# Kernel optimization log

Measured on AMD Instinct MI355X. Metric: run time of the kernel, lower is better.

## Reference

```python
import jax, jax.numpy as jnp
import numpy as np

N_NODES = 50000
N_EDGES = 800000
IN_NODE = 64
IN_EDGE = 32
HIDDEN = 128
NUM_LAYERS = 3
OUT_DIM = 8
NUM_GRAPHS = 128


def setup_inputs() -> dict:
    key = jax.random.key(0)
    ks = jax.random.split(key, 20)
    inp = {
        "x": jax.random.normal(ks[0], (N_NODES, IN_NODE), dtype=jnp.float32),
        "edge_index": jax.random.randint(ks[1], (2, N_EDGES), 0, N_NODES, dtype=jnp.int32),
        "edge_attr": jax.random.normal(ks[2], (N_EDGES, IN_EDGE), dtype=jnp.float32),
        "batch": jnp.sort(jax.random.randint(ks[3], (N_NODES,), 0, NUM_GRAPHS, dtype=jnp.int32)),
    }
    # MLP params per GINEConv layer: Linear(d_in, H) -> ReLU -> Linear(H, H)
    d_ins = [IN_NODE + IN_EDGE] + [HIDDEN + IN_EDGE] * (NUM_LAYERS - 1)
    for i, d_in in enumerate(d_ins):
        inp[f"w{i}_1"] = jax.random.normal(ks[4 + 3 * i], (d_in, HIDDEN), dtype=jnp.float32) * (1.0 / np.sqrt(d_in))
        inp[f"b{i}_1"] = jnp.zeros((HIDDEN,), dtype=jnp.float32)
        inp[f"w{i}_2"] = jax.random.normal(ks[5 + 3 * i], (HIDDEN, HIDDEN), dtype=jnp.float32) * (1.0 / np.sqrt(HIDDEN))
        inp[f"b{i}_2"] = jnp.zeros((HIDDEN,), dtype=jnp.float32)
    inp["lin_w"] = jax.random.normal(ks[15], (HIDDEN, OUT_DIM), dtype=jnp.float32) * (1.0 / np.sqrt(HIDDEN))
    inp["lin_b"] = jnp.zeros((OUT_DIM,), dtype=jnp.float32)
    return inp


def _gine_conv(x, src, dst, edge_attr, w1, b1, w2, b2):
    # gather source node feats, concat with edge feats, 2-layer MLP, scatter-add to dst
    m = jnp.concatenate([x[src], edge_attr], axis=-1)        # [E, d_in]
    h = jax.nn.relu(m @ w1 + b1) @ w2 + b2                   # [E, H]
    return jax.ops.segment_sum(h, dst, num_segments=N_NODES)  # [N, H]


def reference(x, edge_index, edge_attr, batch,
              w0_1, b0_1, w0_2, b0_2,
              w1_1, b1_1, w1_2, b1_2,
              w2_1, b2_1, w2_2, b2_2,
              lin_w, lin_b):
    src, dst = edge_index[0], edge_index[1]
    layers = [(w0_1, b0_1, w0_2, b0_2), (w1_1, b1_1, w1_2, b1_2), (w2_1, b2_1, w2_2, b2_2)]
    h = x
    for (w1, b1, w2, b2) in layers:
        h = jax.nn.relu(_gine_conv(h, src, dst, edge_attr, w1, b1, w2, b2))
    # global mean pool over graphs
    sums = jax.ops.segment_sum(h, batch, num_segments=NUM_GRAPHS)          # [G, H]
    cnts = jax.ops.segment_sum(jnp.ones((N_NODES,), h.dtype), batch, num_segments=NUM_GRAPHS)
    pooled = sums / jnp.maximum(cnts, 1.0)[:, None]
    return pooled @ lin_w + lin_b
```

## Files before the change

kernel.cpp:

```cpp
#include <hip/hip_runtime.h>
#include <hip/hip_bf16.h>
#include <stdint.h>

typedef __attribute__((ext_vector_type(8))) __bf16 bf16x8;
typedef __attribute__((ext_vector_type(4))) __bf16 bf16x4;
typedef __attribute__((ext_vector_type(4))) float f32x4;

static constexpr int NN = 50000;
static constexpr int NE = 800000;
static constexpr int FX = 64;
static constexpr int FE = 32;
static constexpr int H  = 128;
static constexpr int NG = 128;
static constexpr int OD = 8;

__global__ void cvt_f32_bf16(const float* __restrict__ in, __bf16* __restrict__ out, int n) {
  int idx = (blockIdx.x * blockDim.x + threadIdx.x) * 4;
  if (idx + 3 < n) {
    float4 v = *reinterpret_cast<const float4*>(in + idx);
    bf16x4 o;
    o[0] = (__bf16)v.x; o[1] = (__bf16)v.y; o[2] = (__bf16)v.z; o[3] = (__bf16)v.w;
    *reinterpret_cast<bf16x4*>(out + idx) = o;
  } else {
    for (; idx < n; ++idx) out[idx] = (__bf16)in[idx];
  }
}

__global__ void cvt_w_t(const float* __restrict__ w, __bf16* __restrict__ wt, int K) {
  int i = blockIdx.x * blockDim.x + threadIdx.x;
  if (i >= K * 128) return;
  int n = i / K, k = i % K;
  wt[i] = (__bf16)w[k * 128 + n];
}

__global__ void hist_build(const int* __restrict__ dst, int* __restrict__ hist) {
  int e = blockIdx.x * blockDim.x + threadIdx.x;
  if (e < NE) atomicAdd(&hist[dst[e]], 1);
}

__global__ void scan1(const int* __restrict__ hist, int* __restrict__ excl, int* __restrict__ btot) {
  __shared__ int tmp[256];
  int t = threadIdx.x;
  int i = blockIdx.x * 256 + t;
  int v = (i < NN) ? hist[i] : 0;
  tmp[t] = v;
  __syncthreads();
  for (int off = 1; off < 256; off <<= 1) {
    int add = (t >= off) ? tmp[t - off] : 0;
    __syncthreads();
    tmp[t] += add;
    __syncthreads();
  }
  if (i < NN) excl[i] = tmp[t] - v;
  if (t == 255) btot[blockIdx.x] = tmp[255];
}

__global__ void scan2(int* __restrict__ btot, int nb) {
  __shared__ int tmp[256];
  int t = threadIdx.x;
  int v = (t < nb) ? btot[t] : 0;
  tmp[t] = v;
  __syncthreads();
  for (int off = 1; off < 256; off <<= 1) {
    int add = (t >= off) ? tmp[t - off] : 0;
    __syncthreads();
    tmp[t] += add;
    __syncthreads();
  }
  if (t < nb) btot[t] = tmp[t] - v;
}

__global__ void scan3(const int* __restrict__ excl, const int* __restrict__ btot,
                      int* __restrict__ cursor) {
  int i = blockIdx.x * 256 + threadIdx.x;
  if (i < NN) cursor[i] = excl[i] + btot[blockIdx.x];
}

__global__ void scatter_perm(const int* __restrict__ src, const int* __restrict__ dst,
                             int* __restrict__ cursor,
                             int* __restrict__ srcp, int* __restrict__ dstp,
                             int* __restrict__ eperm) {
  int e = blockIdx.x * blockDim.x + threadIdx.x;
  if (e >= NE) return;
  int d = dst[e];
  int p = atomicAdd(&cursor[d], 1);
  srcp[p] = src[e];
  dstp[p] = d;
  eperm[p] = e;
}

__global__ void sort_ea(const float* __restrict__ ea, const int* __restrict__ eperm,
                        __bf16* __restrict__ eabs) {
  int i = blockIdx.x * blockDim.x + threadIdx.x;
  if (i >= NE * 4) return;
  int p = i >> 2, c = i & 3;
  int e = eperm[p];
  float4 v0 = *reinterpret_cast<const float4*>(ea + (size_t)e * FE + c * 8);
  float4 v1 = *reinterpret_cast<const float4*>(ea + (size_t)e * FE + c * 8 + 4);
  bf16x8 o;
  o[0] = (__bf16)v0.x; o[1] = (__bf16)v0.y; o[2] = (__bf16)v0.z; o[3] = (__bf16)v0.w;
  o[4] = (__bf16)v1.x; o[5] = (__bf16)v1.y; o[6] = (__bf16)v1.z; o[7] = (__bf16)v1.w;
  *reinterpret_cast<bf16x8*>(eabs + (size_t)p * FE + c * 8) = o;
}

template<int F, int DIN>
__global__ __launch_bounds__(512) void node_gemm2(
    const __bf16* __restrict__ Ain,
    const __bf16* __restrict__ wt,
    __bf16* __restrict__ Y)
{
  constexpr int APAD = F + 8;
  constexpr int KS   = F / 32;
  constexpr int CH   = F / 8;
  constexpr int AB   = 128 * APAD * 2;
  constexpr int OB   = 128 * 136 * 2;
  constexpr int SB   = (AB > OB) ? AB : OB;
  __shared__ __align__(16) char smem[SB];
  auto As  = reinterpret_cast<__bf16 (*)[APAD]>(smem);
  auto Ost = reinterpret_cast<__bf16 (*)[136]>(smem);

  const int tid   = threadIdx.x;
  const int lane  = tid & 63;
  const int w     = tid >> 6;
  const int m0    = blockIdx.x * 128;
  const int colq  = lane & 15;
  const int krow  = (lane >> 4) * 8;
  const int rbase = (lane >> 4) * 4;
  const int col   = w * 16 + colq;

  bf16x8 bf[KS];
#pragma unroll
  for (int ks = 0; ks < KS; ++ks)
    bf[ks] = *reinterpret_cast<const bf16x8*>(wt + (size_t)col * DIN + ks * 32 + krow);

  for (int i = tid; i < 128 * CH; i += 512) {
    int row = i / CH, c = i % CH;
    int g = m0 + row; if (g >= NN) g = NN - 1;
    *reinterpret_cast<bf16x8*>(&As[row][c * 8]) =
        *reinterpret_cast<const bf16x8*>(Ain + (size_t)g * F + c * 8);
  }
  __syncthreads();

  f32x4 acc[8];
#pragma unroll
  for (int mt = 0; mt < 8; ++mt) acc[mt] = (f32x4){0.f, 0.f, 0.f, 0.f};
#pragma unroll
  for (int ks = 0; ks < KS; ++ks)
#pragma unroll
    for (int mt = 0; mt < 8; ++mt) {
      bf16x8 a = *reinterpret_cast<const bf16x8*>(&As[mt * 16 + colq][ks * 32 + krow]);
      acc[mt] = __builtin_amdgcn_mfma_f32_16x16x32_bf16(a, bf[ks], acc[mt], 0, 0, 0);
    }
  __syncthreads();

#pragma unroll
  for (int mt = 0; mt < 8; ++mt)
#pragma unroll
    for (int r = 0; r < 4; ++r)
      Ost[mt * 16 + rbase + r][col] = (__bf16)acc[mt][r];
  __syncthreads();

  for (int i = tid; i < 128 * 16; i += 512) {
    int row = i >> 4, c = i & 15;
    int g = m0 + row;
    if (g < NN)
      *reinterpret_cast<bf16x8*>(Y + (size_t)g * H + c * 8) =
          *reinterpret_cast<const bf16x8*>(&Ost[row][c * 8]);
  }
}

template<bool WRITE_Y>
__global__ __launch_bounds__(512) void node_wy(
    const float* __restrict__ aggHin,
    const int* __restrict__ deg,
    const __bf16* __restrict__ w2t,
    const float* __restrict__ b2,
    const __bf16* __restrict__ w1t,
    __bf16* __restrict__ Y,
    float* __restrict__ hpre)
{
  __shared__ __bf16 Ast[128][136];
  __shared__ __bf16 Hst[WRITE_Y ? 128 : 1][136];
  __shared__ int deg_s[128];

  const int tid   = threadIdx.x;
  const int lane  = tid & 63;
  const int w     = tid >> 6;
  const int m0    = blockIdx.x * 128;
  const int colq  = lane & 15;
  const int krow  = (lane >> 4) * 8;
  const int rbase = (lane >> 4) * 4;
  const int col   = w * 16 + colq;

  for (int i = tid; i < 128 * 16; i += 512) {
    int row = i >> 4, cb = (i & 15) * 8;
    int g = m0 + row; if (g >= NN) g = NN - 1;
    const float* s = aggHin + (size_t)g * H + cb;
    float4 v0 = *reinterpret_cast<const float4*>(s);
    float4 v1 = *reinterpret_cast<const float4*>(s + 4);
    bf16x8 o;
    o[0] = (__bf16)v0.x; o[1] = (__bf16)v0.y; o[2] = (__bf16)v0.z; o[3] = (__bf16)v0.w;
    o[4] = (__bf16)v1.x; o[5] = (__bf16)v1.y; o[6] = (__bf16)v1.z; o[7] = (__bf16)v1.w;
    *reinterpret_cast<bf16x8*>(&Ast[row][cb]) = o;
  }
  if (tid < 128) {
    int g = m0 + tid;
    deg_s[tid] = (g < NN) ? deg[g] : 0;
  }
  __syncthreads();

  bf16x8 w2f[4];
#pragma unroll
  for (int ks = 0; ks < 4; ++ks)
    w2f[ks] = *reinterpret_cast<const bf16x8*>(w2t + (size_t)col * H + ks * 32 + krow);
  const float b2s = b2[col];

  f32x4 acc[8];
#pragma unroll
  for (int mt = 0; mt < 8; ++mt) acc[mt] = (f32x4){0.f, 0.f, 0.f, 0.f};
#pragma unroll
  for (int ks = 0; ks < 4; ++ks)
#pragma unroll
    for (int mt = 0; mt < 8; ++mt) {
      bf16x8 a = *reinterpret_cast<const bf16x8*>(&Ast[mt * 16 + colq][ks * 32 + krow]);
      acc[mt] = __builtin_amdgcn_mfma_f32_16x16x32_bf16(a, w2f[ks], acc[mt], 0, 0, 0);
    }

  if (WRITE_Y) {
#pragma unroll
    for (int mt = 0; mt < 8; ++mt)
#pragma unroll
      for (int r = 0; r < 4; ++r) {
        int row = mt * 16 + rbase + r;
        float v = acc[mt][r] + (float)deg_s[row] * b2s;
        Hst[row][col] = (__bf16)fmaxf(v, 0.f);
      }
    __syncthreads();

    bf16x8 w1f[4];
#pragma unroll
    for (int ks = 0; ks < 4; ++ks)
      w1f[ks] = *reinterpret_cast<const bf16x8*>(w1t + (size_t)col * 160 + ks * 32 + krow);

    f32x4 acc2[8];
#pragma unroll
    for (int mt = 0; mt < 8; ++mt) acc2[mt] = (f32x4){0.f, 0.f, 0.f, 0.f};
#pragma unroll
    for (int ks = 0; ks < 4; ++ks)
#pragma unroll
      for (int mt = 0; mt < 8; ++mt) {
        bf16x8 a = *reinterpret_cast<const bf16x8*>(&Hst[mt * 16 + colq][ks * 32 + krow]);
        acc2[mt] = __builtin_amdgcn_mfma_f32_16x16x32_bf16(a, w1f[ks], acc2[mt], 0, 0, 0);
      }

#pragma unroll
    for (int mt = 0; mt < 8; ++mt)
#pragma unroll
      for (int r = 0; r < 4; ++r)
        Ast[mt * 16 + rbase + r][col] = (__bf16)acc2[mt][r];
    __syncthreads();

    for (int i = tid; i < 128 * 16; i += 512) {
      int row = i >> 4, cb = (i & 15) * 8;
      int g = m0 + row;
      if (g < NN)
        *reinterpret_cast<bf16x8*>(Y + (size_t)g * H + cb) =
            *reinterpret_cast<const bf16x8*>(&Ast[row][cb]);
    }
  } else {
#pragma unroll
    for (int mt = 0; mt < 8; ++mt)
#pragma unroll
      for (int r = 0; r < 4; ++r) {
        int row = mt * 16 + rbase + r;
        int g = m0 + row;
        if (g < NN)
          hpre[(size_t)g * H + col] = acc[mt][r] + (float)deg_s[row] * b2s;
      }
  }
}

template<int DIN>
__global__ __launch_bounds__(512) void edge_mlp4(
    const __bf16* __restrict__ Yb,
    const __bf16* __restrict__ eabs,
    const int* __restrict__ srcp, const int* __restrict__ dstp,
    const __bf16* __restrict__ w1t,
    const float* __restrict__ b1,
    float* __restrict__ aggH,
    int ntiles)
{
  constexpr int F = DIN - 32;
  constexpr int TPB = 4;
  __shared__ __bf16 Ylds[128][128];
  __shared__ int dst_s[128];

  const int tid   = threadIdx.x;
  const int lane  = tid & 63;
  const int w     = tid >> 6;
  const int colq  = lane & 15;
  const int krow  = (lane >> 4) * 8;
  const int rbase = (lane >> 4) * 4;
  const int col   = w * 16 + colq;

  const bf16x8 b1f = *reinterpret_cast<const bf16x8*>(w1t + (size_t)col * DIN + F + krow);
  const float  b1s = b1[col];

  const int yrow = tid >> 4;
  const int yc   = tid & 15;
  const int drow = tid & 127;

  int t0 = blockIdx.x * TPB;
  int t1 = t0 + TPB; if (t1 > ntiles) t1 = ntiles;
  if (t0 >= ntiles) return;

  int e0 = t0 * 128;
  int sA[4];
#pragma unroll
  for (int k = 0; k < 4; ++k) sA[k] = srcp[e0 + yrow + 32 * k];
  int dreg = dstp[e0 + drow];
  bf16x8 yreg[4];
#pragma unroll
  for (int k = 0; k < 4; ++k)
    yreg[k] = *reinterpret_cast<const bf16x8*>(Yb + (size_t)sA[k] * H + yc * 8);
  bf16x8 aef[8];
#pragma unroll
  for (int mt = 0; mt < 8; ++mt)
    aef[mt] = *reinterpret_cast<const bf16x8*>(eabs + (size_t)(e0 + mt * 16 + colq) * FE + krow);
  {
    int e0n = (t0 + 1 < t1) ? (t0 + 1) * 128 : e0;
#pragma unroll
    for (int k = 0; k < 4; ++k) sA[k] = srcp[e0n + yrow + 32 * k];
  }

  for (int t = t0; t < t1; ++t) {
    __syncthreads();
#pragma unroll
    for (int k = 0; k < 4; ++k) {
      int row = yrow + 32 * k;
      int cb = (yc * 8 + ((row >> 2) & 3) * 16) & 127;
      *reinterpret_cast<bf16x8*>(&Ylds[row][cb]) = yreg[k];
    }
    if (tid < 128) dst_s[tid] = dreg;
    __syncthreads();

    if (t + 1 < t1) {
      int e1 = (t + 1) * 128;
#pragma unroll
      for (int k = 0; k < 4; ++k)
        yreg[k] = *reinterpret_cast<const bf16x8*>(Yb + (size_t)sA[k] * H + yc * 8);
      dreg = dstp[e1 + drow];
      int e2 = (t + 2 < t1) ? (t + 2) * 128 : e1;
#pragma unroll
      for (int k = 0; k < 4; ++k) sA[k] = srcp[e2 + yrow + 32 * k];
    }

    f32x4 acc[8];
#pragma unroll
    for (int mt = 0; mt < 8; ++mt) acc[mt] = (f32x4){b1s, b1s, b1s, b1s};
#pragma unroll
    for (int mt = 0; mt < 8; ++mt)
      acc[mt] = __builtin_amdgcn_mfma_f32_16x16x32_bf16(aef[mt], b1f, acc[mt], 0, 0, 0);

    if (t + 1 < t1) {
      int e1 = (t + 1) * 128;
#pragma unroll
      for (int mt = 0; mt < 8; ++mt)
        aef[mt] = *reinterpret_cast<const bf16x8*>(eabs + (size_t)(e1 + mt * 16 + colq) * FE + krow);
    }

#pragma unroll
    for (int mt = 0; mt < 8; ++mt)
#pragma unroll
      for (int r = 0; r < 4; ++r) {
        int row = mt * 16 + rbase + r;
        int cs = (col + ((row >> 2) & 3) * 16) & 127;
        float v = (float)Ylds[row][cs] + acc[mt][r];
        Ylds[row][cs] = (__bf16)fmaxf(v, 0.f);
      }
    __syncthreads();

    {
      const int rc = tid & 127;
      const int r0 = (tid >> 7) * 32;
      float s = 0.f;
      int d = dst_s[r0];
#pragma unroll 4
      for (int r = r0; r < r0 + 32; ++r) {
        int dn = dst_s[r];
        float v = (float)Ylds[r][(rc + ((r >> 2) & 3) * 16) & 127];
        if (dn != d) { atomicAdd(aggH + (size_t)d * H + rc, s); s = 0.f; d = dn; }
        s += v;
      }
      atomicAdd(aggH + (size_t)d * H + rc, s);
    }
  }
}

__global__ void pool_kernel(const float* __restrict__ agg, const int* __restrict__ batch,
                            float* __restrict__ sums, float* __restrict__ cnts) {
  const int col = threadIdx.x & 127;
  const int sub = threadIdx.x >> 7;
  const int NB = 128;
  int n0 = blockIdx.x * NB + sub * (NB / 2);
  if (n0 >= NN) return;
  int n1 = n0 + NB / 2; if (n1 > NN) n1 = NN;
  float s = 0.f, c = 0.f;
  int g = batch[n0];
  for (int n = n0; n < n1; ++n) {
    int gn = batch[n];
    if (gn != g) {
      atomicAdd(&sums[g * H + col], s);
      if (col == 0) atomicAdd(&cnts[g], c);
      s = 0.f; c = 0.f; g = gn;
    }
    s += fmaxf(agg[(size_t)n * H + col], 0.f);
    c += 1.f;
  }
  atomicAdd(&sums[g * H + col], s);
  if (col == 0) atomicAdd(&cnts[g], c);
}

__global__ void final_kernel(const float* __restrict__ sums, const float* __restrict__ cnts,
                             const float* __restrict__ lw, const float* __restrict__ lb,
                             float* __restrict__ out) {
  int idx = blockIdx.x * blockDim.x + threadIdx.x;
  if (idx >= NG * OD) return;
  int g = idx / OD, o = idx % OD;
  float inv = 1.f / fmaxf(cnts[g], 1.f);
  float s = 0.f;
#pragma unroll 8
  for (int k = 0; k < H; ++k)
    s += sums[g * H + k] * lw[k * OD + o];
  out[idx] = s * inv + lb[o];
}

extern "C" void kernel_launch(void* const* d_in, const int* in_sizes, int n_in,
                              void* d_out, int out_size, void* d_ws, size_t ws_size,
                              hipStream_t stream) {
  const float* x   = (const float*)d_in[0];
  const int*   ei  = (const int*)d_in[1];
  const float* ea  = (const float*)d_in[2];
  const int*   bat = (const int*)d_in[3];
  const float* w1[3] = {(const float*)d_in[4], (const float*)d_in[8],  (const float*)d_in[12]};
  const float* b1[3] = {(const float*)d_in[5], (const float*)d_in[9],  (const float*)d_in[13]};
  const float* w2[3] = {(const float*)d_in[6], (const float*)d_in[10], (const float*)d_in[14]};
  const float* b2[3] = {(const float*)d_in[7], (const float*)d_in[11], (const float*)d_in[15]};
  const float* lw  = (const float*)d_in[16];
  const float* lb  = (const float*)d_in[17];
  float* out = (float*)d_out;

  char* ws = (char*)d_ws;
  size_t off = 0;
  auto alloc = [&](size_t bytes) -> void* {
    void* p = ws + off;
    off = (off + bytes + 255) & ~(size_t)255;
    return p;
  };
  __bf16* xb   = (__bf16*)alloc((size_t)NN * FX * 2);
  __bf16* Yb   = (__bf16*)alloc((size_t)NN * H * 2);
  __bf16* eabs = (__bf16*)alloc((size_t)NE * FE * 2);
  float*  agg  = (float*) alloc((size_t)NN * H * 4);
  __bf16* w1t[3]; __bf16* w2t[3];
  for (int l = 0; l < 3; ++l) {
    w1t[l] = (__bf16*)alloc(128 * 160 * 2);
    w2t[l] = (__bf16*)alloc(128 * 128 * 2);
  }
  float* sums = (float*)alloc(NG * H * 4);
  float* cnts = (float*)alloc(NG * 4);
  int* hist   = (int*)alloc((size_t)NN * 4);
  int* excl   = (int*)alloc((size_t)NN * 4);
  int* btot   = (int*)alloc(256 * 4);
  int* cursor = (int*)alloc((size_t)NN * 4);
  int* srcp   = (int*)alloc((size_t)NE * 4);
  int* dstp   = (int*)alloc((size_t)NE * 4);
  int* eperm  = (int*)alloc((size_t)NE * 4);

  const int* src = ei;
  const int* dst = ei + NE;
  const int NB_SCAN = (NN + 255) / 256;
  const int NTILES = NE / 128;
  const int EGRID  = (NTILES + 3) / 4;
  const int NGRID  = (NN + 127) / 128;

  cvt_f32_bf16<<<(NN * FX / 4 + 255) / 256, 256, 0, stream>>>(x, xb, NN * FX);
  const int dins[3] = {96, 160, 160};
  for (int l = 0; l < 3; ++l) {
    cvt_w_t<<<(dins[l] * 128 + 255) / 256, 256, 0, stream>>>(w1[l], w1t[l], dins[l]);
    cvt_w_t<<<(128 * 128 + 255) / 256, 256, 0, stream>>>(w2[l], w2t[l], 128);
  }

  hipMemsetAsync(hist, 0, (size_t)NN * 4, stream);
  hist_build<<<(NE + 255) / 256, 256, 0, stream>>>(dst, hist);
  scan1<<<NB_SCAN, 256, 0, stream>>>(hist, excl, btot);
  scan2<<<1, 256, 0, stream>>>(btot, NB_SCAN);
  scan3<<<NB_SCAN, 256, 0, stream>>>(excl, btot, cursor);
  scatter_perm<<<(NE + 255) / 256, 256, 0, stream>>>(src, dst, cursor, srcp, dstp, eperm);
  sort_ea<<<(NE * 4 + 255) / 256, 256, 0, stream>>>(ea, eperm, eabs);

  node_gemm2<64, 96><<<NGRID, 512, 0, stream>>>(xb, w1t[0], Yb);
  hipMemsetAsync(agg, 0, (size_t)NN * H * 4, stream);
  edge_mlp4<96><<<EGRID, 512, 0, stream>>>(Yb, eabs, srcp, dstp, w1t[0], b1[0], agg, NTILES);

  for (int l = 1; l < 3; ++l) {
    node_wy<true><<<NGRID, 512, 0, stream>>>(agg, hist, w2t[l - 1], b2[l - 1],
                                             w1t[l], Yb, nullptr);
    hipMemsetAsync(agg, 0, (size_t)NN * H * 4, stream);
    edge_mlp4<160><<<EGRID, 512, 0, stream>>>(Yb, eabs, srcp, dstp, w1t[l], b1[l], agg, NTILES);
  }

  node_wy<false><<<NGRID, 512, 0, stream>>>(agg, hist, w2t[2], b2[2],
                                            nullptr, nullptr, agg);
  hipMemsetAsync(sums, 0, NG * H * 4, stream);
  hipMemsetAsync(cnts, 0, NG * 4, stream);
  pool_kernel<<<(NN + 127) / 128, 256, 0, stream>>>(agg, bat, sums, cnts);
  final_kernel<<<(NG * OD + 255) / 256, 256, 0, stream>>>(sums, cnts, lw, lb, out);
}
```

Baseline: 481.4 us.

## Partition edge MLP by destination node ranges with LDS-local aggregation

Replaces the fixed edge-tile partition with a CSR rowptr-based split where each block owns 32 destination nodes and processes all of their incoming edges. Partial sums are reduced in shared memory with LDS atomics and written once to global memory. This removes the global float atomics and the per-layer memset of the aggregation buffer. The cost is load imbalance across blocks (variable edge counts), a larger LDS footprint that may reduce occupancy, and removal of the Ylds swizzle (padding to 132 used instead).

```diff
diff --git a/kernel.cpp b/kernel.cpp
--- a/kernel.cpp
+++ b/kernel.cpp
@@ -13,6 +13,7 @@
 static constexpr int H  = 128;
 static constexpr int NG = 128;
 static constexpr int OD = 8;
+static constexpr int NPB = 32;
 
 __global__ void cvt_f32_bf16(const float* __restrict__ in, __bf16* __restrict__ out, int n) {
   int idx = (blockIdx.x * blockDim.x + threadIdx.x) * 4;
@@ -71,9 +72,14 @@
 }
 
 __global__ void scan3(const int* __restrict__ excl, const int* __restrict__ btot,
-                      int* __restrict__ cursor) {
+                      int* __restrict__ cursor, int* __restrict__ rowptr) {
   int i = blockIdx.x * 256 + threadIdx.x;
-  if (i < NN) cursor[i] = excl[i] + btot[blockIdx.x];
+  if (i < NN) {
+    int v = excl[i] + btot[blockIdx.x];
+    cursor[i] = v;
+    rowptr[i] = v;
+  }
+  if (blockIdx.x == 0 && threadIdx.x == 0) rowptr[NN] = NE;
 }
 
 __global__ void scatter_perm(const int* __restrict__ src, const int* __restrict__ dst,
@@ -281,19 +287,19 @@
 }
 
 template<int DIN>
-__global__ __launch_bounds__(512) void edge_mlp4(
+__global__ __launch_bounds__(512) void edge_mlp5(
     const __bf16* __restrict__ Yb,
     const __bf16* __restrict__ eabs,
     const int* __restrict__ srcp, const int* __restrict__ dstp,
+    const int* __restrict__ rowptr,
     const __bf16* __restrict__ w1t,
     const float* __restrict__ b1,
-    float* __restrict__ aggH,
-    int ntiles)
+    float* __restrict__ aggH)
 {
   constexpr int F = DIN - 32;
-  constexpr int TPB = 4;
-  __shared__ __bf16 Ylds[128][128];
-  __shared__ int dst_s[128];
+  __shared__ __bf16 Ylds[128][132];
+  __shared__ float  agg_l[33][132];
+  __shared__ int    nl_s[128];
 
   const int tid   = threadIdx.x;
   const int lane  = tid & 63;
@@ -303,6 +309,15 @@
   const int rbase = (lane >> 4) * 4;
   const int col   = w * 16 + colq;
 
+  const int nb0 = blockIdx.x * NPB;
+  const int nb1 = (nb0 + NPB < NN) ? nb0 + NPB : NN;
+  const int eb0 = rowptr[nb0];
+  const int eb1 = rowptr[nb1];
+  const int ntb = (eb1 - eb0 + 127) >> 7;
+
+  for (int i = tid; i < 33 * 132; i += 512)
+    (&agg_l[0][0])[i] = 0.f;
+
   const bf16x8 b1f = *reinterpret_cast<const bf16x8*>(w1t + (size_t)col * DIN + F + krow);
   const float  b1s = b1[col];
 
@@ -310,90 +325,123 @@
   const int yc   = tid & 15;
   const int drow = tid & 127;
 
-  int t0 = blockIdx.x * TPB;
-  int t1 = t0 + TPB; if (t1 > ntiles) t1 = ntiles;
-  if (t0 >= ntiles) return;
-
-  int e0 = t0 * 128;
-  int sA[4];
-#pragma unroll
-  for (int k = 0; k < 4; ++k) sA[k] = srcp[e0 + yrow + 32 * k];
-  int dreg = dstp[e0 + drow];
-  bf16x8 yreg[4];
-#pragma unroll
-  for (int k = 0; k < 4; ++k)
-    yreg[k] = *reinterpret_cast<const bf16x8*>(Yb + (size_t)sA[k] * H + yc * 8);
-  bf16x8 aef[8];
-#pragma unroll
-  for (int mt = 0; mt < 8; ++mt)
-    aef[mt] = *reinterpret_cast<const bf16x8*>(eabs + (size_t)(e0 + mt * 16 + colq) * FE + krow);
-  {
-    int e0n = (t0 + 1 < t1) ? (t0 + 1) * 128 : e0;
-#pragma unroll
-    for (int k = 0; k < 4; ++k) sA[k] = srcp[e0n + yrow + 32 * k];
-  }
-
-  for (int t = t0; t < t1; ++t) {
-    __syncthreads();
+  if (ntb > 0) {
+    int sA[4];
 #pragma unroll
     for (int k = 0; k < 4; ++k) {
-      int row = yrow + 32 * k;
-      int cb = (yc * 8 + ((row >> 2) & 3) * 16) & 127;
-      *reinterpret_cast<bf16x8*>(&Ylds[row][cb]) = yreg[k];
-    }
-    if (tid < 128) dst_s[tid] = dreg;
-    __syncthreads();
-
-    if (t + 1 < t1) {
-      int e1 = (t + 1) * 128;
+      int e = eb0 + yrow + 32 * k; if (e > NE - 1) e = NE - 1;
+      sA[k] = srcp[e];
+    }
+    int dreg;
+    { int e = eb0 + drow; if (e > NE - 1) e = NE - 1; dreg = dstp[e]; }
+    bf16x8 yreg[4];
+#pragma unroll
+    for (int k = 0; k < 4; ++k)
+      yreg[k] = *reinterpret_cast<const bf16x8*>(Yb + (size_t)sA[k] * H + yc * 8);
+    bf16x8 aef[8];
+#pragma unroll
+    for (int mt = 0; mt < 8; ++mt) {
+      int e = eb0 + mt * 16 + colq; if (e > NE - 1) e = NE - 1;
+      aef[mt] = *reinterpret_cast<const bf16x8*>(eabs + (size_t)e * FE + krow);
+    }
+    {
+      int e1 = eb0 + ((1 < ntb) ? 128 : 0);
+#pragma unroll
+      for (int k = 0; k < 4; ++k) {
+        int e = e1 + yrow + 32 * k; if (e > NE - 1) e = NE - 1;
+        sA[k] = srcp[e];
+      }
+    }
+
+    for (int t = 0; t < ntb; ++t) {
+      __syncthreads();
 #pragma unroll
       for (int k = 0; k < 4; ++k)
-        yreg[k] = *reinterpret_cast<const bf16x8*>(Yb + (size_t)sA[k] * H + yc * 8);
-      dreg = dstp[e1 + drow];
-      int e2 = (t + 2 < t1) ? (t + 2) * 128 : e1;
-#pragma unroll
-      for (int k = 0; k < 4; ++k) sA[k] = srcp[e2 + yrow + 32 * k];
-    }
-
-    f32x4 acc[8];
-#pragma unroll
-    for (int mt = 0; mt < 8; ++mt) acc[mt] = (f32x4){b1s, b1s, b1s, b1s};
-#pragma unroll
-    for (int mt = 0; mt < 8; ++mt)
-      acc[mt] = __builtin_amdgcn_mfma_f32_16x16x32_bf16(aef[mt], b1f, acc[mt], 0, 0, 0);
-
-    if (t + 1 < t1) {
-      int e1 = (t + 1) * 128;
+        *reinterpret_cast<bf16x8*>(&Ylds[yrow + 32 * k][yc * 8]) = yreg[k];
+      if (tid < 128) {
+        int e = eb0 + t * 128 + tid;
+        nl_s[tid] = (e < eb1) ? (dreg - nb0) : 32;
+      }
+      __syncthreads();
+
+      if (t + 1 < ntb) {
+        int e1 = eb0 + (t + 1) * 128;
+#pragma unroll
+        for (int k = 0; k < 4; ++k)
+          yreg[k] = *reinterpret_cast<const bf16x8*>(Yb + (size_t)sA[k] * H + yc * 8);
+        { int e = e1 + drow; if (e > NE - 1) e = NE - 1; dreg = dstp[e]; }
+        int e2 = eb0 + ((t + 2 < ntb) ? (t + 2) : (t + 1)) * 128;
+#pragma unroll
+        for (int k = 0; k < 4; ++k) {
+          int e = e2 + yrow + 32 * k; if (e > NE - 1) e = NE - 1;
+          sA[k] = srcp[e];
+        }
+      }
+
+      f32x4 acc[8];
+#pragma unroll
+      for (int mt = 0; mt < 8; ++mt) acc[mt] = (f32x4){b1s, b1s, b1s, b1s};
 #pragma unroll
       for (int mt = 0; mt < 8; ++mt)
-        aef[mt] = *reinterpret_cast<const bf16x8*>(eabs + (size_t)(e1 + mt * 16 + colq) * FE + krow);
-    }
-
-#pragma unroll
-    for (int mt = 0; mt < 8; ++mt)
-#pragma unroll
-      for (int r = 0; r < 4; ++r) {
-        int row = mt * 16 + rbase + r;
-        int cs = (col + ((row >> 2) & 3) * 16) & 127;
-        float v = (float)Ylds[row][cs] + acc[mt][r];
-        Ylds[row][cs] = (__bf16)fmaxf(v, 0.f);
-      }
-    __syncthreads();
-
-    {
-      const int rc = tid & 127;
-      const int r0 = (tid >> 7) * 32;
-      float s = 0.f;
-      int d = dst_s[r0];
-#pragma unroll 4
-      for (int r = r0; r < r0 + 32; ++r) {
-        int dn = dst_s[r];
-        float v = (float)Ylds[r][(rc + ((r >> 2) & 3) * 16) & 127];
-        if (dn != d) { atomicAdd(aggH + (size_t)d * H + rc, s); s = 0.f; d = dn; }
-        s += v;
-      }
-      atomicAdd(aggH + (size_t)d * H + rc, s);
-    }
+        acc[mt] = __builtin_amdgcn_mfma_f32_16x16x32_bf16(aef[mt], b1f, acc[mt], 0, 0, 0);
+
+      if (t + 1 < ntb) {
+        int e1 = eb0 + (t + 1) * 128;
+#pragma unroll
+        for (int mt = 0; mt < 8; ++mt) {
+          int e = e1 + mt * 16 + colq; if (e > NE - 1) e = NE - 1;
+          aef[mt] = *reinterpret_cast<const bf16x8*>(eabs + (size_t)e * FE + krow);
+        }
+      }
+
+#pragma unroll
+      for (int mt = 0; mt < 8; ++mt)
+#pragma unroll
+        for (int r = 0; r < 4; ++r) {
+          int row = mt * 16 + rbase + r;
+          float v = (float)Ylds[row][col] + acc[mt][r];
+          Ylds[row][col] = (__bf16)fmaxf(v, 0.f);
+        }
+      __syncthreads();
+
+      {
+        const int rg = tid >> 4;
+        const int ch = tid & 15;
+        const int r0 = rg * 4;
+        float vs[8];
+#pragma unroll
+        for (int j = 0; j < 8; ++j) vs[j] = 0.f;
+        int cur = nl_s[r0];
+#pragma unroll
+        for (int j = 0; j < 4; ++j) {
+          const int rr = r0 + j;
+          const int nl = nl_s[rr];
+          bf16x8 yv = *reinterpret_cast<const bf16x8*>(&Ylds[rr][ch * 8]);
+          if (nl != cur) {
+#pragma unroll
+            for (int jj = 0; jj < 8; ++jj) {
+              atomicAdd(&agg_l[cur][ch * 8 + jj], vs[jj]);
+              vs[jj] = 0.f;
+            }
+            cur = nl;
+          }
+#pragma unroll
+          for (int jj = 0; jj < 8; ++jj) vs[jj] += (float)yv[jj];
+        }
+#pragma unroll
+        for (int jj = 0; jj < 8; ++jj)
+          atomicAdd(&agg_l[cur][ch * 8 + jj], vs[jj]);
+      }
+    }
+  }
+  __syncthreads();
+
+  for (int i = tid; i < NPB * 32; i += 512) {
+    int row = i >> 5, c4 = (i & 31) * 4;
+    int g = nb0 + row;
+    if (g < NN)
+      *reinterpret_cast<float4*>(aggH + (size_t)g * H + c4) =
+          *reinterpret_cast<const float4*>(&agg_l[row][c4]);
   }
 }
 
@@ -472,6 +520,7 @@
   int* excl   = (int*)alloc((size_t)NN * 4);
   int* btot   = (int*)alloc(256 * 4);
   int* cursor = (int*)alloc((size_t)NN * 4);
+  int* rowptr = (int*)alloc((size_t)(NN + 1) * 4);
   int* srcp   = (int*)alloc((size_t)NE * 4);
   int* dstp   = (int*)alloc((size_t)NE * 4);
   int* eperm  = (int*)alloc((size_t)NE * 4);
@@ -479,8 +528,7 @@
   const int* src = ei;
   const int* dst = ei + NE;
   const int NB_SCAN = (NN + 255) / 256;
-  const int NTILES = NE / 128;
-  const int EGRID  = (NTILES + 3) / 4;
+  const int EGRID  = (NN + NPB - 1) / NPB;
   const int NGRID  = (NN + 127) / 128;
 
   cvt_f32_bf16<<<(NN * FX / 4 + 255) / 256, 256, 0, stream>>>(x, xb, NN * FX);
@@ -494,19 +542,19 @@
   hist_build<<<(NE + 255) / 256, 256, 0, stream>>>(dst, hist);
   scan1<<<NB_SCAN, 256, 0, stream>>>(hist, excl, btot);
   scan2<<<1, 256, 0, stream>>>(btot, NB_SCAN);
-  scan3<<<NB_SCAN, 256, 0, stream>>>(excl, btot, cursor);
+  scan3<<<NB_SCAN, 256, 0, stream>>>(excl, btot, cursor, rowptr);
   scatter_perm<<<(NE + 255) / 256, 256, 0, stream>>>(src, dst, cursor, srcp, dstp, eperm);
   sort_ea<<<(NE * 4 + 255) / 256, 256, 0, stream>>>(ea, eperm, eabs);
 
   node_gemm2<64, 96><<<NGRID, 512, 0, stream>>>(xb, w1t[0], Yb);
-  hipMemsetAsync(agg, 0, (size_t)NN * H * 4, stream);
-  edge_mlp4<96><<<EGRID, 512, 0, stream>>>(Yb, eabs, srcp, dstp, w1t[0], b1[0], agg, NTILES);
+  edge_mlp5<96><<<EGRID, 512, 0, stream>>>(Yb, eabs, srcp, dstp, rowptr,
+                                           w1t[0], b1[0], agg);
 
   for (int l = 1; l < 3; ++l) {
     node_wy<true><<<NGRID, 512, 0, stream>>>(agg, hist, w2t[l - 1], b2[l - 1],
                                              w1t[l], Yb, nullptr);
-    hipMemsetAsync(agg, 0, (size_t)NN * H * 4, stream);
-    edge_mlp4<160><<<EGRID, 512, 0, stream>>>(Yb, eabs, srcp, dstp, w1t[l], b1[l], agg, NTILES);
+    edge_mlp5<160><<<EGRID, 512, 0, stream>>>(Yb, eabs, srcp, dstp, rowptr,
+                                              w1t[l], b1[l], agg);
   }
 
   node_wy<false><<<NGRID, 512, 0, stream>>>(agg, hist, w2t[2], b2[2],
```

Measured after the change: 955.7 us. 1.99x slower.
